# Optimization experiments

Measured on AMD Instinct MI355X. Metric: run time of the kernel, lower is better.

The kernel has to match this reference:

```python
import jax, jax.numpy as jnp
import numpy as np

NUM_HEADS = 8
FREQ_RATIO = 0.5


def _resize_bilinear(img, out_h, out_w):
    """Bilinear resize of last two dims, matching torch interpolate align_corners=False."""
    in_h, in_w = img.shape[-2], img.shape[-1]

    def idx(in_size, out_size):
        src = jnp.maximum((jnp.arange(out_size, dtype=jnp.float32) + 0.5) * (in_size / out_size) - 0.5, 0.0)
        i0 = jnp.floor(src).astype(jnp.int32)
        i1 = jnp.minimum(i0 + 1, in_size - 1)
        w = src - i0.astype(jnp.float32)
        return i0, i1, w

    r0, r1, wr = idx(in_h, out_h)
    img = img[..., r0, :] * (1.0 - wr)[:, None] + img[..., r1, :] * wr[:, None]
    c0, c1, wc = idx(in_w, out_w)
    img = img[..., c0] * (1.0 - wc) + img[..., c1] * wc
    return img


def setup_inputs() -> dict:
    key = jax.random.key(0)
    ks = jax.random.split(key, 6)
    B, T, J, C = 4, 256, 17, 512
    H = NUM_HEADS
    x = jax.random.normal(ks[0], (B, T, J, C), dtype=jnp.float32)
    att_map = jax.random.uniform(ks[1], (B, H, J, T, T), dtype=jnp.float32)
    weight = jax.random.uniform(ks[2], (1,), dtype=jnp.float32)
    w_qkv = jax.random.normal(ks[3], (C, 3 * C), dtype=jnp.float32) * 0.02
    w_proj = jax.random.normal(ks[4], (C, C), dtype=jnp.float32) * 0.02
    b_proj = jnp.zeros((C,), dtype=jnp.float32)
    freq_gate = jnp.ones((1,), dtype=jnp.float32)
    return {"x": x, "att_map": att_map, "weight": weight, "w_qkv": w_qkv,
            "w_proj": w_proj, "b_proj": b_proj, "freq_gate": freq_gate}


def reference(x, att_map, weight, w_qkv, w_proj, b_proj, freq_gate):
    B, T, J, C = x.shape
    H = NUM_HEADS
    d = C // H
    scale = d ** (-0.5)

    qkv = (x @ w_qkv).reshape(B, T, J, 3, H, d)
    qkv = jnp.transpose(qkv, (3, 0, 4, 2, 1, 5))  # [3,B,H,J,T,d]
    q, k, v = qkv[0], qkv[1], qkv[2]

    # time-domain attention over T, per (B,H,J)
    attn_time = jax.nn.softmax(jnp.einsum('bhjtd,bhjsd->bhjts', q, k) * scale, axis=-1)

    # frequency-domain attention
    qf = jnp.fft.rfft(q, axis=3)
    kf = jnp.fft.rfft(k, axis=3)
    F = qf.shape[3]                      # T//2 + 1
    keep = max(1, int(F * FREQ_RATIO))
    qf = qf[:, :, :, :keep]
    kf = kf[:, :, :, :keep]
    af = jnp.einsum('bhjfd,bhjgd->bhjfg', qf, jnp.conj(kf)) * scale  # complex [B,H,J,keep,keep]
    # torch combines softmax(real) + 1j*softmax(imag); only the real part survives
    af_real = jax.nn.softmax(af.real, axis=-1)
    af_real = jnp.pad(af_real, ((0, 0), (0, 0), (0, 0), (0, F - keep), (0, 0)))  # zero-pad rows to F
    attn_freq = _resize_bilinear(af_real, T, T)  # [B,H,J,T,T]

    gate = jax.nn.sigmoid(freq_gate)  # broadcastable scalar
    attn_self = gate * attn_freq + (1.0 - gate) * attn_time
    attn = weight * attn_self + (1.0 - weight) * att_map

    out = jnp.einsum('bhjts,bhjsd->bhjtd', attn, v)        # [B,H,J,T,d]
    out = jnp.transpose(out, (0, 3, 2, 1, 4)).reshape(B, T, J, C)
    return out @ w_proj + b_proj
```

## Files before the change

### kernel.cpp

```cpp
#include <hip/hip_runtime.h>
#include <hip/hip_bf16.h>


#define SCALE 0.125f
#define LSTR 72

typedef __attribute__((ext_vector_type(4))) float f32x4;
typedef __attribute__((ext_vector_type(8))) short bf16x8;
typedef __attribute__((ext_vector_type(8))) unsigned short u16x8;

__device__ __forceinline__ float bf2f(unsigned short u) {
  return __uint_as_float(((unsigned int)u) << 16);
}
__device__ __forceinline__ unsigned short f2bf(float f) {
  unsigned int u = __float_as_uint(f);
  u += 0x7FFFu + ((u >> 16) & 1u);
  return (unsigned short)(u >> 16);
}

__global__ __launch_bounds__(256) void conv_x(
    const float* __restrict__ x, unsigned short* __restrict__ xh,
    unsigned short* __restrict__ xl) {
  const size_t i = ((size_t)blockIdx.x * 256 + threadIdx.x) * 8;
  float4 a = *(const float4*)(x + i);
  float4 b = *(const float4*)(x + i + 4);
  float vv[8] = {a.x, a.y, a.z, a.w, b.x, b.y, b.z, b.w};
  u16x8 hi, lo;
#pragma unroll
  for (int e = 0; e < 8; ++e) {
    unsigned short h = f2bf(vv[e]);
    hi[e] = h;
    lo[e] = f2bf(vv[e] - bf2f(h));
  }
  *(u16x8*)&xh[i] = hi;
  *(u16x8*)&xl[i] = lo;
}

__global__ __launch_bounds__(256) void conv_wT(
    const float* __restrict__ w, unsigned short* __restrict__ th,
    unsigned short* __restrict__ tl, int N) {
  __shared__ float T[64][65];
  const int tid = threadIdx.x;
  const int nt = blockIdx.x * 64, kt = blockIdx.y * 64;
  for (int i = tid; i < 4096; i += 256) {
    const int r = i >> 6, c = i & 63;
    T[r][c] = w[(size_t)(kt + r) * N + nt + c];
  }
  __syncthreads();
  for (int i = tid; i < 4096; i += 256) {
    const int rn = i >> 6, ck = i & 63;
    const float v = T[ck][rn];
    const unsigned short h = f2bf(v);
    const size_t o = (size_t)(nt + rn) * 512 + kt + ck;
    th[o] = h;
    tl[o] = f2bf(v - bf2f(h));
  }
}

__global__ __launch_bounds__(256, 2) void qkv_gemm(
    const unsigned short* __restrict__ xh, const unsigned short* __restrict__ xl,
    const unsigned short* __restrict__ wh, const unsigned short* __restrict__ wl,
    unsigned short* __restrict__ qh, unsigned short* __restrict__ ql,
    unsigned short* __restrict__ kh, unsigned short* __restrict__ kl,
    unsigned short* __restrict__ vh) {
  __shared__ __attribute__((aligned(16))) unsigned short Wt[2][128 * LSTR];
  __shared__ __attribute__((aligned(16))) unsigned short Xt[2][128 * LSTR];

  const int tid = threadIdx.x;
  const int bx = blockIdx.x, by = blockIdx.y;
  const int wid = tid >> 6, lane = tid & 63;
  const int lr = lane & 15, lg = lane >> 4;
  const int wr = wid >> 1, wc = wid & 1;
  const int srow = tid >> 3, skg = tid & 7;

  const unsigned short* xhp = xh + (size_t)(by * 128 + srow) * 512 + skg * 8;
  const unsigned short* xlp = xl + (size_t)(by * 128 + srow) * 512 + skg * 8;
  const unsigned short* whp = wh + (size_t)(bx * 128 + srow) * 512 + skg * 8;
  const unsigned short* wlp = wl + (size_t)(bx * 128 + srow) * 512 + skg * 8;

  u16x8 rxh[4], rxl[4], rwh[4], rwl[4];
  auto loadk = [&](int k0) {
#pragma unroll
    for (int it = 0; it < 4; ++it) {
      const size_t o = (size_t)(32 * it) * 512 + k0;
      rxh[it] = *(const u16x8*)(xhp + o);
      rxl[it] = *(const u16x8*)(xlp + o);
      rwh[it] = *(const u16x8*)(whp + o);
      rwl[it] = *(const u16x8*)(wlp + o);
    }
  };

  f32x4 acc[4][4];
#pragma unroll
  for (int nt = 0; nt < 4; ++nt)
#pragma unroll
    for (int mt = 0; mt < 4; ++mt) acc[nt][mt] = (f32x4){0.f, 0.f, 0.f, 0.f};

  loadk(0);
  for (int s = 0; s < 8; ++s) {
    if (s) __syncthreads();
#pragma unroll
    for (int it = 0; it < 4; ++it) {
      const int base = (srow + 32 * it) * LSTR + skg * 8;
      *(u16x8*)&Xt[0][base] = rxh[it];
      *(u16x8*)&Xt[1][base] = rxl[it];
      *(u16x8*)&Wt[0][base] = rwh[it];
      *(u16x8*)&Wt[1][base] = rwl[it];
    }
    __syncthreads();
    if (s < 7) loadk((s + 1) * 64);
#pragma unroll
    for (int kh2 = 0; kh2 < 2; ++kh2) {
      const int kbase = kh2 * 32 + lg * 8;
      bf16x8 Ah[4], Al[4], Bh[4], Bl[4];
#pragma unroll
      for (int nt = 0; nt < 4; ++nt) {
        const int n = wr * 64 + nt * 16 + lr;
        Ah[nt] = *(bf16x8*)&Wt[0][n * LSTR + kbase];
        Al[nt] = *(bf16x8*)&Wt[1][n * LSTR + kbase];
      }
#pragma unroll
      for (int mt = 0; mt < 4; ++mt) {
        const int m = wc * 64 + mt * 16 + lr;
        Bh[mt] = *(bf16x8*)&Xt[0][m * LSTR + kbase];
        Bl[mt] = *(bf16x8*)&Xt[1][m * LSTR + kbase];
      }
#pragma unroll
      for (int nt = 0; nt < 4; ++nt)
#pragma unroll
        for (int mt = 0; mt < 4; ++mt) {
          acc[nt][mt] = __builtin_amdgcn_mfma_f32_16x16x32_bf16(Ah[nt], Bh[mt], acc[nt][mt], 0, 0, 0);
          acc[nt][mt] = __builtin_amdgcn_mfma_f32_16x16x32_bf16(Ah[nt], Bl[mt], acc[nt][mt], 0, 0, 0);
          acc[nt][mt] = __builtin_amdgcn_mfma_f32_16x16x32_bf16(Al[nt], Bh[mt], acc[nt][mt], 0, 0, 0);
        }
    }
  }

#pragma unroll
  for (int mt = 0; mt < 4; ++mt) {
    const int m = by * 128 + wc * 64 + mt * 16 + lr;
    const int jj = m % 17;
    const int bt = m / 17;
    const int t = bt & 255;
    const int b = bt >> 8;
#pragma unroll
    for (int nt = 0; nt < 4; ++nt) {
      const int c = bx * 128 + wr * 64 + nt * 16 + lg * 4;
      const int qi = c >> 9;
      const int h = (c >> 6) & 7;
      const int dd = c & 63;
      const size_t base = ((size_t)((b * 8 + h) * 17 + jj)) * 16384 + t * 64 + dd;
      float a0 = acc[nt][mt][0], a1 = acc[nt][mt][1], a2 = acc[nt][mt][2],
            a3 = acc[nt][mt][3];
      ushort4 hi4 = make_ushort4(f2bf(a0), f2bf(a1), f2bf(a2), f2bf(a3));
      if (qi == 2) {
        *(ushort4*)&vh[base] = hi4;
      } else {
        ushort4 lo4 = make_ushort4(f2bf(a0 - bf2f(hi4.x)), f2bf(a1 - bf2f(hi4.y)),
                                   f2bf(a2 - bf2f(hi4.z)), f2bf(a3 - bf2f(hi4.w)));
        unsigned short* dh = qi ? kh : qh;
        unsigned short* dl = qi ? kl : ql;
        *(ushort4*)&dh[base] = hi4;
        *(ushort4*)&dl[base] = lo4;
      }
    }
  }
}

__global__ __launch_bounds__(256) void freq_kernel(
    const unsigned short* __restrict__ qhp, const unsigned short* __restrict__ qlp,
    const unsigned short* __restrict__ khp, const unsigned short* __restrict__ klp,
    unsigned short* __restrict__ af_out) {
  __shared__ __attribute__((aligned(16))) unsigned short qT[2][64 * 256];
  __shared__ __attribute__((aligned(16))) unsigned short QF[4][64 * 64];
  __shared__ __attribute__((aligned(16))) unsigned short KF[4][64 * 64];

  const int tid = threadIdx.x;
  const int head = blockIdx.x;
  const int w = tid >> 6, lane = tid & 63;
  const int lr = lane & 15, lg = lane >> 4;
  const int f0 = w << 4;

  bf16x8 Ech[8], Ecl[8], Esh[8], Esl[8];
  {
    const int f = f0 + lr;
#pragma unroll
    for (int kb = 0; kb < 8; ++kb) {
      bf16x8 ch, cl, sh, sl;
#pragma unroll
      for (int i = 0; i < 8; ++i) {
        int t = kb * 32 + lg * 8 + i;
        int idx = (f * t) & 255;
        float s, c;
        __sincosf((float)idx * 0.02454369260617026f, &s, &c);
        unsigned short chh = f2bf(c);
        unsigned short shh = f2bf(s);
        ch[i] = (short)chh;
        cl[i] = (short)f2bf(c - bf2f(chh));
        sh[i] = (short)shh;
        sl[i] = (short)f2bf(s - bf2f(shh));
      }
      Ech[kb] = ch; Ecl[kb] = cl; Esh[kb] = sh; Esl[kb] = sl;
    }
  }

  for (int pass = 0; pass < 2; ++pass) {
    const unsigned short* sh_ = (pass ? khp : qhp) + head * 16384;
    const unsigned short* sl_ = (pass ? klp : qlp) + head * 16384;
    __syncthreads();
    for (int i = tid; i < 4096; i += 256) {
      int t = i >> 4, dq = i & 15;
      ushort4 hv = *(const ushort4*)&sh_[t * 64 + dq * 4];
      ushort4 lv = *(const ushort4*)&sl_[t * 64 + dq * 4];
      unsigned short hvv[4] = {hv.x, hv.y, hv.z, hv.w};
      unsigned short lvv[4] = {lv.x, lv.y, lv.z, lv.w};
#pragma unroll
      for (int c = 0; c < 4; ++c) {
        int d = dq * 4 + c;
        int byo = d * 512 + ((t * 2) ^ ((d & 31) << 4));
        *(unsigned short*)((char*)qT[0] + byo) = hvv[c];
        *(unsigned short*)((char*)qT[1] + byo) = lvv[c];
      }
    }
    __syncthreads();

    f32x4 ar[4], ai[4];
#pragma unroll
    for (int nt = 0; nt < 4; ++nt) {
      ar[nt] = (f32x4){0.f, 0.f, 0.f, 0.f};
      ai[nt] = (f32x4){0.f, 0.f, 0.f, 0.f};
    }
#pragma unroll
    for (int kb = 0; kb < 8; ++kb) {
#pragma unroll
      for (int nt = 0; nt < 4; ++nt) {
        const int d = nt * 16 + lr;
        const int byo = d * 512 + ((kb * 64 + lg * 16) ^ ((d & 31) << 4));
        bf16x8 bh = *(bf16x8*)((char*)qT[0] + byo);
        bf16x8 bl = *(bf16x8*)((char*)qT[1] + byo);
        ar[nt] = __builtin_amdgcn_mfma_f32_16x16x32_bf16(Ech[kb], bh, ar[nt], 0, 0, 0);
        ar[nt] = __builtin_amdgcn_mfma_f32_16x16x32_bf16(Ech[kb], bl, ar[nt], 0, 0, 0);
        ar[nt] = __builtin_amdgcn_mfma_f32_16x16x32_bf16(Ecl[kb], bh, ar[nt], 0, 0, 0);
        ai[nt] = __builtin_amdgcn_mfma_f32_16x16x32_bf16(Esh[kb], bh, ai[nt], 0, 0, 0);
        ai[nt] = __builtin_amdgcn_mfma_f32_16x16x32_bf16(Esh[kb], bl, ai[nt], 0, 0, 0);
        ai[nt] = __builtin_amdgcn_mfma_f32_16x16x32_bf16(Esl[kb], bh, ai[nt], 0, 0, 0);
      }
    }
    unsigned short(*DST)[64 * 64] = pass ? KF : QF;
#pragma unroll
    for (int nt = 0; nt < 4; ++nt) {
#pragma unroll
      for (int j = 0; j < 4; ++j) {
        const int f = f0 + lg * 4 + j;
        const int d = nt * 16 + lr;
        const int byo = f * 128 + ((d * 2) ^ ((f & 7) << 4));
        float vr = ar[nt][j], vi = ai[nt][j];
        unsigned short rh = f2bf(vr);
        unsigned short ih = f2bf(vi);
        *(unsigned short*)((char*)DST[0] + byo) = rh;
        *(unsigned short*)((char*)DST[1] + byo) = f2bf(vr - bf2f(rh));
        *(unsigned short*)((char*)DST[2] + byo) = ih;
        *(unsigned short*)((char*)DST[3] + byo) = f2bf(vi - bf2f(ih));
      }
    }
  }
  __syncthreads();

  f32x4 acc[4];
#pragma unroll
  for (int nt = 0; nt < 4; ++nt) acc[nt] = (f32x4){0.f, 0.f, 0.f, 0.f};
#pragma unroll
  for (int kb = 0; kb < 2; ++kb) {
    const int fA = f0 + lr;
    const int abyo = fA * 128 + ((kb * 64 + lg * 16) ^ ((fA & 7) << 4));
    bf16x8 arh = *(bf16x8*)((char*)QF[0] + abyo);
    bf16x8 arl = *(bf16x8*)((char*)QF[1] + abyo);
    bf16x8 aih = *(bf16x8*)((char*)QF[2] + abyo);
    bf16x8 ail = *(bf16x8*)((char*)QF[3] + abyo);
#pragma unroll
    for (int nt = 0; nt < 4; ++nt) {
      const int g = nt * 16 + lr;
      const int bbyo = g * 128 + ((kb * 64 + lg * 16) ^ ((g & 7) << 4));
      bf16x8 brh = *(bf16x8*)((char*)KF[0] + bbyo);
      bf16x8 brl = *(bf16x8*)((char*)KF[1] + bbyo);
      bf16x8 bih = *(bf16x8*)((char*)KF[2] + bbyo);
      bf16x8 bil = *(bf16x8*)((char*)KF[3] + bbyo);
      acc[nt] = __builtin_amdgcn_mfma_f32_16x16x32_bf16(arh, brh, acc[nt], 0, 0, 0);
      acc[nt] = __builtin_amdgcn_mfma_f32_16x16x32_bf16(arh, brl, acc[nt], 0, 0, 0);
      acc[nt] = __builtin_amdgcn_mfma_f32_16x16x32_bf16(arl, brh, acc[nt], 0, 0, 0);
      acc[nt] = __builtin_amdgcn_mfma_f32_16x16x32_bf16(aih, bih, acc[nt], 0, 0, 0);
      acc[nt] = __builtin_amdgcn_mfma_f32_16x16x32_bf16(aih, bil, acc[nt], 0, 0, 0);
      acc[nt] = __builtin_amdgcn_mfma_f32_16x16x32_bf16(ail, bih, acc[nt], 0, 0, 0);
    }
  }

  unsigned short* outh = af_out + head * 4096;
#pragma unroll
  for (int j = 0; j < 4; ++j) {
    float m = fmaxf(fmaxf(acc[0][j], acc[1][j]), fmaxf(acc[2][j], acc[3][j]));
#pragma unroll
    for (int mask = 1; mask < 16; mask <<= 1) m = fmaxf(m, __shfl_xor(m, mask));
    float e[4];
    float rs = 0.f;
#pragma unroll
    for (int nt = 0; nt < 4; ++nt) {
      e[nt] = __expf((acc[nt][j] - m) * SCALE);
      rs += e[nt];
    }
#pragma unroll
    for (int mask = 1; mask < 16; mask <<= 1) rs += __shfl_xor(rs, mask);
    const float inv = 1.0f / rs;
    const int f = f0 + lg * 4 + j;
#pragma unroll
    for (int nt = 0; nt < 4; ++nt) outh[f * 64 + nt * 16 + lr] = f2bf(e[nt] * inv);
  }
}

__global__ __launch_bounds__(256) void attn_kernel(
    const unsigned short* __restrict__ qhp, const unsigned short* __restrict__ khp,
    const unsigned short* __restrict__ vhp, const unsigned short* __restrict__ af,
    const float* __restrict__ att_map, const float* __restrict__ weight,
    const float* __restrict__ fgate, float* __restrict__ out_perm) {
  __shared__ unsigned short Ks[256 * 64];
  __shared__ unsigned short Vt[64 * 256];
  __shared__ unsigned short afl[64 * 66];
  __shared__ unsigned short Psc[4][16 * 40];

  const int tid = threadIdx.x;
  const int head = blockIdx.x;
  const int jj = head % 17;
  const int hb = head / 17;
  const int h = hb & 7;
  const int b = hb >> 3;
  const int w = tid >> 6, lane = tid & 63;
  const int lr = lane & 15, lg = lane >> 4;

  const float* amh = att_map + (size_t)head * 65536;
  const unsigned short* qbase = qhp + head * 16384;

  bf16x8 rq[2];
  {
    const unsigned short* qrow = qbase + (w * 64 + lr) * 64 + lg * 8;
    rq[0] = *(const bf16x8*)(qrow);
    rq[1] = *(const bf16x8*)(qrow + 32);
  }

  const unsigned short* ksrc = khp + head * 16384;
  const unsigned short* vsrc = vhp + head * 16384;
  for (int i = tid; i < 2048; i += 256) {
    int s = i >> 3, dq8 = i & 7;
    u16x8 kv = *(const u16x8*)&ksrc[s * 64 + dq8 * 8];
    int koff = s * 128 + ((dq8 * 16) ^ ((s & 7) << 4));
    *(u16x8*)((char*)Ks + koff) = kv;
  }
  for (int i = tid; i < 4096; i += 256) {
    int s = i >> 4, dq = i & 15;
    ushort4 v4 = *(const ushort4*)&vsrc[s * 64 + dq * 4];
    unsigned short vv[4] = {v4.x, v4.y, v4.z, v4.w};
#pragma unroll
    for (int c = 0; c < 4; ++c) {
      int d = dq * 4 + c;
      int voff = d * 512 + ((s * 2) ^ ((d & 7) << 4));
      *(unsigned short*)((char*)Vt + voff) = vv[c];
    }
  }
  const unsigned short* asrc = af + head * 4096;
  for (int i = tid; i < 1024; i += 256) {
    int f = i >> 4, gq = (i & 15) << 2;
    *(ushort4*)&afl[f * 66 + gq] = *(const ushort4*)&asrc[f * 64 + gq];
  }
  __syncthreads();

  const float wv = weight[0];
  const float gate = 1.0f / (1.0f + __expf(-fgate[0]));
  unsigned short* psc = Psc[w];

  for (int tt = 0; tt < 4; ++tt) {
    const int tw = w * 64 + tt * 16;

    bf16x8 aq[2] = {rq[0], rq[1]};

    f32x4 S[16];
#pragma unroll
    for (int nt = 0; nt < 16; ++nt) {
      f32x4 accv = {0.f, 0.f, 0.f, 0.f};
#pragma unroll
      for (int kc = 0; kc < 2; ++kc) {
        int srow = nt * 16 + lr;
        int d0 = kc * 32 + lg * 8;
        int off = srow * 128 + ((d0 * 2) ^ ((srow & 7) << 4));
        bf16x8 bk = *(bf16x8*)((char*)Ks + off);
        accv = __builtin_amdgcn_mfma_f32_16x16x32_bf16(aq[kc], bk, accv, 0, 0, 0);
      }
      S[nt] = accv;
    }

    if (tt < 3) {
      const unsigned short* qrow = qbase + (tw + 16 + lr) * 64 + lg * 8;
      rq[0] = *(const bf16x8*)(qrow);
      rq[1] = *(const bf16x8*)(qrow + 32);
    }

    float inv[4], mrow[4];
#pragma unroll
    for (int j = 0; j < 4; ++j) {
      float m = -1e30f;
#pragma unroll
      for (int nt = 0; nt < 16; ++nt) m = fmaxf(m, S[nt][j]);
#pragma unroll
      for (int mask = 1; mask < 16; mask <<= 1) m = fmaxf(m, __shfl_xor(m, mask));
      mrow[j] = m;
    }
#pragma unroll
    for (int j = 0; j < 4; ++j) {
      float rs = 0.f;
#pragma unroll
      for (int nt = 0; nt < 16; ++nt) {
        float e = __expf((S[nt][j] - mrow[j]) * SCALE);
        S[nt][j] = e;
        rs += e;
      }
#pragma unroll
      for (int mask = 1; mask < 16; mask <<= 1) rs += __shfl_xor(rs, mask);
      inv[j] = 1.0f / rs;
    }

#pragma unroll
    for (int j = 0; j < 4; ++j) {
      const int t = tw + lg * 4 + j;
      float srcf = fmaxf((t + 0.5f) * (129.0f / 256.0f) - 0.5f, 0.0f);
      int f0r = (int)srcf;
      float wf = srcf - (float)f0r;
      int f1r = f0r + 1;
      if (f1r > 128) f1r = 128;
      const bool v0 = (f0r < 64), v1 = (f1r < 64);
#pragma unroll
      for (int nt = 0; nt < 16; ++nt) {
        const int s = nt * 16 + lr;
        float am = amh[t * 256 + s];
        float srcg = fmaxf((s + 0.5f) * 0.25f - 0.5f, 0.0f);
        int g0 = (int)srcg;
        float wc = srcg - (float)g0;
        int g1 = g0 + 1;
        if (g1 > 63) g1 = 63;
        float fr = 0.f;
        if (v0)
          fr += (1.0f - wf) *
                (bf2f(afl[f0r * 66 + g0]) * (1.0f - wc) + bf2f(afl[f0r * 66 + g1]) * wc);
        if (v1)
          fr += wf *
                (bf2f(afl[f1r * 66 + g0]) * (1.0f - wc) + bf2f(afl[f1r * 66 + g1]) * wc);
        float pt = S[nt][j] * inv[j];
        S[nt][j] = wv * (gate * fr + (1.0f - gate) * pt) + (1.0f - wv) * am;
      }
    }

    f32x4 O[4];
#pragma unroll
    for (int dt = 0; dt < 4; ++dt) O[dt] = (f32x4){0.f, 0.f, 0.f, 0.f};
#pragma unroll
    for (int sb = 0; sb < 8; ++sb) {
#pragma unroll
      for (int half = 0; half < 2; ++half) {
        const int nt = sb * 2 + half;
#pragma unroll
        for (int j = 0; j < 4; ++j) {
          psc[(lg * 4 + j) * 40 + half * 16 + lr] = f2bf(S[nt][j]);
        }
      }
      bf16x8 pa = *(bf16x8*)&psc[lr * 40 + lg * 8];
#pragma unroll
      for (int dt = 0; dt < 4; ++dt) {
        int d = dt * 16 + lr;
        int s0 = sb * 32 + lg * 8;
        int off = d * 512 + ((s0 * 2) ^ ((d & 7) << 4));
        bf16x8 bv = *(bf16x8*)((char*)Vt + off);
        O[dt] = __builtin_amdgcn_mfma_f32_16x16x32_bf16(pa, bv, O[dt], 0, 0, 0);
      }
    }

#pragma unroll
    for (int j = 0; j < 4; ++j) {
      const int t = tw + lg * 4 + j;
      float* orow = out_perm + ((size_t)((b * 256 + t) * 17 + jj)) * 512 + h * 64;
#pragma unroll
      for (int dt = 0; dt < 4; ++dt) {
        orow[dt * 16 + lr] = O[dt][j];
      }
    }
  }
}

__global__ __launch_bounds__(256, 2) void proj_gemm(
    const float* __restrict__ A,
    const unsigned short* __restrict__ wh, const unsigned short* __restrict__ wl,
    const float* __restrict__ bias, float* __restrict__ out) {
  __shared__ __attribute__((aligned(16))) unsigned short Wt[2][128 * LSTR];
  __shared__ __attribute__((aligned(16))) unsigned short Xt[2][128 * LSTR];

  const int tid = threadIdx.x;
  const int bx = blockIdx.x, by = blockIdx.y;
  const int wid = tid >> 6, lane = tid & 63;
  const int lr = lane & 15, lg = lane >> 4;
  const int wr = wid >> 1, wc = wid & 1;
  const int srow = tid >> 3, skg = tid & 7;

  const float* ap = A + (size_t)(by * 128 + srow) * 512 + skg * 8;
  const unsigned short* whp = wh + (size_t)(bx * 128 + srow) * 512 + skg * 8;
  const unsigned short* wlp = wl + (size_t)(bx * 128 + srow) * 512 + skg * 8;

  float4 rA[4][2];
  u16x8 rwh[4], rwl[4];
  auto loadk = [&](int k0) {
#pragma unroll
    for (int it = 0; it < 4; ++it) {
      const size_t o = (size_t)(32 * it) * 512 + k0;
      rA[it][0] = *(const float4*)(ap + o);
      rA[it][1] = *(const float4*)(ap + o + 4);
      rwh[it] = *(const u16x8*)(whp + o);
      rwl[it] = *(const u16x8*)(wlp + o);
    }
  };

  f32x4 acc[4][4];
#pragma unroll
  for (int nt = 0; nt < 4; ++nt)
#pragma unroll
    for (int mt = 0; mt < 4; ++mt) acc[nt][mt] = (f32x4){0.f, 0.f, 0.f, 0.f};

  loadk(0);
  for (int s = 0; s < 8; ++s) {
    if (s) __syncthreads();
#pragma unroll
    for (int it = 0; it < 4; ++it) {
      const int base = (srow + 32 * it) * LSTR + skg * 8;
      float vv[8] = {rA[it][0].x, rA[it][0].y, rA[it][0].z, rA[it][0].w,
                     rA[it][1].x, rA[it][1].y, rA[it][1].z, rA[it][1].w};
      u16x8 hi, lo;
#pragma unroll
      for (int e = 0; e < 8; ++e) {
        unsigned short h = f2bf(vv[e]);
        hi[e] = h;
        lo[e] = f2bf(vv[e] - bf2f(h));
      }
      *(u16x8*)&Xt[0][base] = hi;
      *(u16x8*)&Xt[1][base] = lo;
      *(u16x8*)&Wt[0][base] = rwh[it];
      *(u16x8*)&Wt[1][base] = rwl[it];
    }
    __syncthreads();
    if (s < 7) loadk((s + 1) * 64);
#pragma unroll
    for (int kh2 = 0; kh2 < 2; ++kh2) {
      const int kbase = kh2 * 32 + lg * 8;
      bf16x8 Ah[4], Al[4], Bh[4], Bl[4];
#pragma unroll
      for (int nt = 0; nt < 4; ++nt) {
        const int n = wr * 64 + nt * 16 + lr;
        Ah[nt] = *(bf16x8*)&Wt[0][n * LSTR + kbase];
        Al[nt] = *(bf16x8*)&Wt[1][n * LSTR + kbase];
      }
#pragma unroll
      for (int mt = 0; mt < 4; ++mt) {
        const int m = wc * 64 + mt * 16 + lr;
        Bh[mt] = *(bf16x8*)&Xt[0][m * LSTR + kbase];
        Bl[mt] = *(bf16x8*)&Xt[1][m * LSTR + kbase];
      }
#pragma unroll
      for (int nt = 0; nt < 4; ++nt)
#pragma unroll
        for (int mt = 0; mt < 4; ++mt) {
          acc[nt][mt] = __builtin_amdgcn_mfma_f32_16x16x32_bf16(Ah[nt], Bh[mt], acc[nt][mt], 0, 0, 0);
          acc[nt][mt] = __builtin_amdgcn_mfma_f32_16x16x32_bf16(Ah[nt], Bl[mt], acc[nt][mt], 0, 0, 0);
          acc[nt][mt] = __builtin_amdgcn_mfma_f32_16x16x32_bf16(Al[nt], Bh[mt], acc[nt][mt], 0, 0, 0);
        }
    }
  }

#pragma unroll
  for (int mt = 0; mt < 4; ++mt) {
    const int m = by * 128 + wc * 64 + mt * 16 + lr;
#pragma unroll
    for (int nt = 0; nt < 4; ++nt) {
      const int n = bx * 128 + wr * 64 + nt * 16 + lg * 4;
      float4 bi = *(const float4*)&bias[n];
      *(float4*)&out[(size_t)m * 512 + n] =
          make_float4(acc[nt][mt][0] + bi.x, acc[nt][mt][1] + bi.y,
                      acc[nt][mt][2] + bi.z, acc[nt][mt][3] + bi.w);
    }
  }
}

extern "C" void kernel_launch(void* const* d_in, const int* in_sizes, int n_in,
                              void* d_out, int out_size, void* d_ws, size_t ws_size,
                              hipStream_t stream) {
  (void)in_sizes; (void)n_in; (void)out_size; (void)ws_size;
  const float* x = (const float*)d_in[0];
  const float* att_map = (const float*)d_in[1];
  const float* weight = (const float*)d_in[2];
  const float* w_qkv = (const float*)d_in[3];
  const float* w_proj = (const float*)d_in[4];
  const float* b_proj = (const float*)d_in[5];
  const float* fgate = (const float*)d_in[6];
  float* out = (float*)d_out;

  char* ws = (char*)d_ws;
  const size_t PB = 17825792;
  unsigned short* qh = (unsigned short*)(ws);
  unsigned short* ql = (unsigned short*)(ws + PB);
  unsigned short* kh = (unsigned short*)(ws + 2 * PB);
  unsigned short* kl = (unsigned short*)(ws + 3 * PB);
  unsigned short* vh = (unsigned short*)(ws + 4 * PB);
  unsigned short* af = (unsigned short*)(ws + 5 * PB);
  char* base = ws + 5 * PB + 4456448;
  unsigned short* xh = (unsigned short*)(base);
  unsigned short* xl = (unsigned short*)(base + PB);
  float* out_perm = (float*)(base);
  unsigned short* wqh = (unsigned short*)(base + 35651584);
  unsigned short* wql = (unsigned short*)(base + 35651584 + 1572864);
  unsigned short* wph = (unsigned short*)(base + 35651584 + 2 * 1572864);
  unsigned short* wpl = (unsigned short*)(base + 35651584 + 2 * 1572864 + 524288);

  conv_x<<<4352, 256, 0, stream>>>(x, xh, xl);
  conv_wT<<<dim3(24, 8), 256, 0, stream>>>(w_qkv, wqh, wql, 1536);
  conv_wT<<<dim3(8, 8), 256, 0, stream>>>(w_proj, wph, wpl, 512);
  qkv_gemm<<<dim3(12, 136), 256, 0, stream>>>(xh, xl, wqh, wql, qh, ql, kh, kl, vh);
  freq_kernel<<<544, 256, 0, stream>>>(qh, ql, kh, kl, af);
  attn_kernel<<<544, 256, 0, stream>>>(qh, kh, vh, af, att_map, weight, fgate,
                                       out_perm);
  proj_gemm<<<dim3(4, 136), 256, 0, stream>>>(out_perm, wph, wpl, b_proj, out);
}
```

Before: 396.6 us.

## Write V transposed from QKV GEMM and read it directly from global in attention

The QKV GEMM epilogue now stores V in a [d][t] transposed layout per head, so the attention kernel no longer builds a transposed V tile in shared memory and reads its MFMA B operands straight from global memory. This frees 32KB of LDS per block, and the launch bound is raised to allow three blocks per CU for more occupancy. The cost is scattered 2-byte global stores in the GEMM epilogue and repeated global or cache reads of V inside the inner loop instead of LDS reads.

```diff
diff --git a/kernel.cpp b/kernel.cpp
--- a/kernel.cpp
+++ b/kernel.cpp
@@ -62,7 +62,7 @@
     const unsigned short* __restrict__ wh, const unsigned short* __restrict__ wl,
     unsigned short* __restrict__ qh, unsigned short* __restrict__ ql,
     unsigned short* __restrict__ kh, unsigned short* __restrict__ kl,
-    unsigned short* __restrict__ vh) {
+    unsigned short* __restrict__ vt) {
   __shared__ __attribute__((aligned(16))) unsigned short Wt[2][128 * LSTR];
   __shared__ __attribute__((aligned(16))) unsigned short Xt[2][128 * LSTR];
 
@@ -149,19 +149,22 @@
       const int qi = c >> 9;
       const int h = (c >> 6) & 7;
       const int dd = c & 63;
-      const size_t base = ((size_t)((b * 8 + h) * 17 + jj)) * 16384 + t * 64 + dd;
+      const size_t hdbase = ((size_t)((b * 8 + h) * 17 + jj)) * 16384;
       float a0 = acc[nt][mt][0], a1 = acc[nt][mt][1], a2 = acc[nt][mt][2],
             a3 = acc[nt][mt][3];
       ushort4 hi4 = make_ushort4(f2bf(a0), f2bf(a1), f2bf(a2), f2bf(a3));
       if (qi == 2) {
-        *(ushort4*)&vh[base] = hi4;
+        vt[hdbase + (size_t)(dd + 0) * 256 + t] = hi4.x;
+        vt[hdbase + (size_t)(dd + 1) * 256 + t] = hi4.y;
+        vt[hdbase + (size_t)(dd + 2) * 256 + t] = hi4.z;
+        vt[hdbase + (size_t)(dd + 3) * 256 + t] = hi4.w;
       } else {
         ushort4 lo4 = make_ushort4(f2bf(a0 - bf2f(hi4.x)), f2bf(a1 - bf2f(hi4.y)),
                                    f2bf(a2 - bf2f(hi4.z)), f2bf(a3 - bf2f(hi4.w)));
         unsigned short* dh = qi ? kh : qh;
         unsigned short* dl = qi ? kl : ql;
-        *(ushort4*)&dh[base] = hi4;
-        *(ushort4*)&dl[base] = lo4;
+        *(ushort4*)&dh[hdbase + t * 64 + dd] = hi4;
+        *(ushort4*)&dl[hdbase + t * 64 + dd] = lo4;
       }
     }
   }
@@ -316,13 +319,12 @@
   }
 }
 
-__global__ __launch_bounds__(256) void attn_kernel(
+__global__ __launch_bounds__(256, 3) void attn_kernel(
     const unsigned short* __restrict__ qhp, const unsigned short* __restrict__ khp,
-    const unsigned short* __restrict__ vhp, const unsigned short* __restrict__ af,
+    const unsigned short* __restrict__ vtp, const unsigned short* __restrict__ af,
     const float* __restrict__ att_map, const float* __restrict__ weight,
     const float* __restrict__ fgate, float* __restrict__ out_perm) {
   __shared__ unsigned short Ks[256 * 64];
-  __shared__ unsigned short Vt[64 * 256];
   __shared__ unsigned short afl[64 * 66];
   __shared__ unsigned short Psc[4][16 * 40];
 
@@ -337,6 +339,7 @@
 
   const float* amh = att_map + (size_t)head * 65536;
   const unsigned short* qbase = qhp + head * 16384;
+  const unsigned short* vtb = vtp + head * 16384;
 
   bf16x8 rq[2];
   {
@@ -346,23 +349,11 @@
   }
 
   const unsigned short* ksrc = khp + head * 16384;
-  const unsigned short* vsrc = vhp + head * 16384;
   for (int i = tid; i < 2048; i += 256) {
     int s = i >> 3, dq8 = i & 7;
     u16x8 kv = *(const u16x8*)&ksrc[s * 64 + dq8 * 8];
     int koff = s * 128 + ((dq8 * 16) ^ ((s & 7) << 4));
     *(u16x8*)((char*)Ks + koff) = kv;
-  }
-  for (int i = tid; i < 4096; i += 256) {
-    int s = i >> 4, dq = i & 15;
-    ushort4 v4 = *(const ushort4*)&vsrc[s * 64 + dq * 4];
-    unsigned short vv[4] = {v4.x, v4.y, v4.z, v4.w};
-#pragma unroll
-    for (int c = 0; c < 4; ++c) {
-      int d = dq * 4 + c;
-      int voff = d * 512 + ((s * 2) ^ ((d & 7) << 4));
-      *(unsigned short*)((char*)Vt + voff) = vv[c];
-    }
   }
   const unsigned short* asrc = af + head * 4096;
   for (int i = tid; i < 1024; i += 256) {
@@ -469,12 +460,11 @@
         }
       }
       bf16x8 pa = *(bf16x8*)&psc[lr * 40 + lg * 8];
+      const int s0 = sb * 32 + lg * 8;
 #pragma unroll
       for (int dt = 0; dt < 4; ++dt) {
-        int d = dt * 16 + lr;
-        int s0 = sb * 32 + lg * 8;
-        int off = d * 512 + ((s0 * 2) ^ ((d & 7) << 4));
-        bf16x8 bv = *(bf16x8*)((char*)Vt + off);
+        const int d = dt * 16 + lr;
+        bf16x8 bv = *(const bf16x8*)&vtb[d * 256 + s0];
         O[dt] = __builtin_amdgcn_mfma_f32_16x16x32_bf16(pa, bv, O[dt], 0, 0, 0);
       }
     }
@@ -610,7 +600,7 @@
   unsigned short* ql = (unsigned short*)(ws + PB);
   unsigned short* kh = (unsigned short*)(ws + 2 * PB);
   unsigned short* kl = (unsigned short*)(ws + 3 * PB);
-  unsigned short* vh = (unsigned short*)(ws + 4 * PB);
+  unsigned short* vt = (unsigned short*)(ws + 4 * PB);
   unsigned short* af = (unsigned short*)(ws + 5 * PB);
   char* base = ws + 5 * PB + 4456448;
   unsigned short* xh = (unsigned short*)(base);
@@ -624,9 +614,9 @@
   conv_x<<<4352, 256, 0, stream>>>(x, xh, xl);
   conv_wT<<<dim3(24, 8), 256, 0, stream>>>(w_qkv, wqh, wql, 1536);
   conv_wT<<<dim3(8, 8), 256, 0, stream>>>(w_proj, wph, wpl, 512);
-  qkv_gemm<<<dim3(12, 136), 256, 0, stream>>>(xh, xl, wqh, wql, qh, ql, kh, kl, vh);
+  qkv_gemm<<<dim3(12, 136), 256, 0, stream>>>(xh, xl, wqh, wql, qh, ql, kh, kl, vt);
   freq_kernel<<<544, 256, 0, stream>>>(qh, ql, kh, kl, af);
-  attn_kernel<<<544, 256, 0, stream>>>(qh, kh, vh, af, att_map, weight, fgate,
+  attn_kernel<<<544, 256, 0, stream>>>(qh, kh, vt, af, att_map, weight, fgate,
                                        out_perm);
   proj_gemm<<<dim3(4, 136), 256, 0, stream>>>(out_perm, wph, wpl, b_proj, out);
 }
```

Measured after the change: 850.4 us. +114.4%, slower.
